# Performance work log

Measured on AMD Instinct MI355X. Metric: run time of the kernel, lower is better.

The kernel has to match this reference:

```python
import jax, jax.numpy as jnp
import numpy as np

N_HEADS, D_MODEL, D_HEAD = 12, 768, 64
INIT_RANGE = 0.02
IGNORE = -100000.0

def setup_inputs() -> dict:
    key = jax.random.key(0)
    ks = jax.random.split(key, 5)
    x = jax.random.normal(ks[0], (4, 2048, D_MODEL), dtype=jnp.float32)
    W_Q = jax.random.normal(ks[1], (N_HEADS, D_MODEL, D_HEAD), dtype=jnp.float32) * INIT_RANGE
    W_K = jax.random.normal(ks[2], (N_HEADS, D_MODEL, D_HEAD), dtype=jnp.float32) * INIT_RANGE
    W_V = jax.random.normal(ks[3], (N_HEADS, D_MODEL, D_HEAD), dtype=jnp.float32) * INIT_RANGE
    W_O = jax.random.normal(ks[4], (N_HEADS, D_HEAD, D_MODEL), dtype=jnp.float32) * INIT_RANGE
    b_Q = jnp.zeros((N_HEADS, D_HEAD), dtype=jnp.float32)
    b_K = jnp.zeros((N_HEADS, D_HEAD), dtype=jnp.float32)
    b_V = jnp.zeros((N_HEADS, D_HEAD), dtype=jnp.float32)
    b_O = jnp.zeros((D_MODEL,), dtype=jnp.float32)
    return {"normalized_resid_pre": x, "W_Q": W_Q, "b_Q": b_Q, "W_K": W_K,
            "b_K": b_K, "W_V": W_V, "b_V": b_V, "W_O": W_O, "b_O": b_O}

def reference(normalized_resid_pre, W_Q, b_Q, W_K, b_K, W_V, b_V, W_O, b_O):
    x = normalized_resid_pre  # [b, s, d_model]
    q = jnp.einsum('bsd,hde->bshe', x, W_Q) + b_Q  # [b, s, h, d_head]
    k = jnp.einsum('bsd,hde->bshe', x, W_K) + b_K
    v = jnp.einsum('bsd,hde->bshe', x, W_V) + b_V
    scores = jnp.einsum('bqhe,bkhe->bhqk', q, k) / jnp.sqrt(jnp.float32(D_HEAD))
    S = x.shape[1]
    causal = jnp.triu(jnp.ones((S, S), dtype=bool), k=1)  # True above diagonal
    scores = jnp.where(causal, jnp.float32(IGNORE), scores)
    pattern = jax.nn.softmax(scores, axis=-1)  # [b, h, q, k]
    z = jnp.einsum('bhqk,bkhe->bqhe', pattern, v)
    attn_out = jnp.einsum('bqhe,hed->bqd', z, W_O) + b_O
    return attn_out
```

## Files before the change

### kernel.cpp

```cpp
#include <hip/hip_runtime.h>

typedef unsigned short u16;
typedef __bf16 bf16x8 __attribute__((ext_vector_type(8)));
typedef float f32x4 __attribute__((ext_vector_type(4)));

#define D_MODEL 768
#define NH 12
#define SEQ 2048
#define BB 4
#define QSCALE 0.18033688011112042f
#define FIXM 8.0f

__device__ __forceinline__ u16 f2b(float f) {
  __bf16 h = (__bf16)f;
  return __builtin_bit_cast(u16, h);
}

__device__ __forceinline__ void gload16(const void* g, void* l) {
  __builtin_amdgcn_global_load_lds((__attribute__((address_space(1))) void*)g,
                                   (__attribute__((address_space(3))) void*)l, 16, 0, 0);
}

__device__ __forceinline__ f32x4 mm16(bf16x8 a, bf16x8 b, f32x4 c) {
  return __builtin_amdgcn_mfma_f32_16x16x32_bf16(a, b, c, 0, 0, 0);
}

__global__ void prep_kernel(const float* __restrict__ x, const float* __restrict__ wq,
                            const float* __restrict__ wk, const float* __restrict__ wv,
                            const float* __restrict__ wo, const float* __restrict__ bq,
                            const float* __restrict__ bk, const float* __restrict__ bv,
                            u16* __restrict__ xb, u16* __restrict__ wt,
                            u16* __restrict__ wot, float* __restrict__ qkvb) {
  const int bid = blockIdx.x;
  if (bid < 6144) {
    int i = (bid * 256 + threadIdx.x) * 4;
    float4 v = *(const float4*)&x[i];
    ushort4 o;
    o.x = f2b(v.x); o.y = f2b(v.y); o.z = f2b(v.z); o.w = f2b(v.w);
    *(ushort4*)&xb[i] = o;
  } else {
    int i = (bid - 6144) * 256 + threadIdx.x;
    {
      int cp = i / 768, d = i % 768;
      int proj = cp / 768, c = cp % 768, h = c / 64, e = c % 64;
      const float* W = (proj == 0) ? wq : ((proj == 1) ? wk : wv);
      float v = W[(size_t)h * 49152 + d * 64 + e];
      if (proj == 0) v *= QSCALE;
      wt[i] = f2b(v);
    }
    if (i < 768 * 768) {
      int rp = i / 768, d = i % 768;
      wot[i] = f2b(wo[(size_t)d * 768 + rp]);
    }
    if (i < 2304) {
      int proj = i / 768, c = i % 768;
      float v = (proj == 0) ? bq[c] * QSCALE : ((proj == 1) ? bk[c] : bv[c]);
      qkvb[i] = v;
    }
  }
}

__global__ __launch_bounds__(512) void gemm_qkv_kernel(
    const u16* __restrict__ A, const u16* __restrict__ Bt,
    const float* __restrict__ qkvb, u16* __restrict__ qw, u16* __restrict__ kw,
    u16* __restrict__ vw) {
  __shared__ u16 lds[73728];
  const int tid = threadIdx.x;
  const int w = tid >> 6, lane = tid & 63;
  const int lg = lane >> 4, cl = lane & 15;
  const int L = blockIdx.x;
  const int v = (L & 7) * 72 + (L >> 3);
  const int bm = v % 9, bn = v / 9;
  const int wr = w >> 1, wc = w & 1;
  const int NT = 12;

  f32x4 vzero = {0.f, 0.f, 0.f, 0.f};
  f32x4 acc[4][4];
#pragma unroll
  for (int mi = 0; mi < 4; mi++)
#pragma unroll
    for (int ni = 0; ni < 4; ni++) acc[mi][ni] = vzero;

  const u16* aB = A + (size_t)bm * 256 * D_MODEL;
  const u16* bB = Bt + (size_t)bn * 128 * D_MODEL;
  const int l8 = lane >> 3, l7 = lane & 7;

  auto stage = [&](int buf, int kt, int half) {
    const int kof = kt * 64;
#pragma unroll
    for (int j2 = 0; j2 < 2; j2++) {
      const int r0 = (w * 4 + half * 2 + j2) * 8;
      gload16(aB + (size_t)(r0 + l8) * D_MODEL + kof + l7 * 8,
              &lds[buf * 16384 + r0 * 64]);
    }
    const int r0b = (w * 2 + half) * 8;
    gload16(bB + (size_t)(r0b + l8) * D_MODEL + kof + l7 * 8,
            &lds[49152 + buf * 8192 + r0b * 64]);
  };

  stage(0, 0, 0); stage(0, 0, 1);
  stage(1, 1, 0); stage(1, 1, 1);
  asm volatile("s_waitcnt vmcnt(6)" ::: "memory");
  __builtin_amdgcn_s_barrier();

  for (int kt = 0; kt < NT; ++kt) {
    const int cA = (kt % 3) * 16384;
    const int cB = 49152 + (kt % 3) * 8192;
    const int nbuf = (kt + 2) % 3;
#pragma unroll
    for (int ks = 0; ks < 2; ks++) {
      bf16x8 af[4], bf4[4];
#pragma unroll
      for (int mi = 0; mi < 4; mi++)
        af[mi] = *(const bf16x8*)&lds[cA + (wr * 64 + mi * 16 + cl) * 64 + ks * 32 + lg * 8];
#pragma unroll
      for (int ni = 0; ni < 4; ni++)
        bf4[ni] = *(const bf16x8*)&lds[cB + (wc * 64 + ni * 16 + cl) * 64 + ks * 32 + lg * 8];
      if (kt + 2 < NT) stage(nbuf, kt + 2, ks);
      if (ks == 1) {
        if (kt + 2 < NT) asm volatile("s_waitcnt vmcnt(6)" ::: "memory");
        else asm volatile("s_waitcnt vmcnt(0)" ::: "memory");
      }
      __builtin_amdgcn_s_barrier();
      __builtin_amdgcn_s_setprio(1);
#pragma unroll
      for (int mi = 0; mi < 4; mi++)
#pragma unroll
        for (int ni = 0; ni < 4; ni++)
          acc[mi][ni] = mm16(af[mi], bf4[ni], acc[mi][ni]);
      __builtin_amdgcn_s_setprio(0);
      __builtin_amdgcn_s_barrier();
    }
  }

  __syncthreads();
  u16* lw = &lds[w * 4096];
  const int cm = bm * 256 + wr * 64;
  const int cn = bn * 128 + wc * 64;
  const int proj = cm / 768;
  const int h = (cm % 768) >> 6;
  const int b = cn >> 11, s_base = cn & 2047;
  const int rlo = lane >> 3, q8 = lane & 7;

  float bz[4][4];
#pragma unroll
  for (int mi = 0; mi < 4; mi++) {
    float4 b4 = *(const float4*)&qkvb[cm + mi * 16 + lg * 4];
    bz[mi][0] = b4.x; bz[mi][1] = b4.y; bz[mi][2] = b4.z; bz[mi][3] = b4.w;
  }

  if (proj < 2) {
#pragma unroll
    for (int mi = 0; mi < 4; mi++) {
      const int e0 = mi * 16 + lg * 4;
#pragma unroll
      for (int ni = 0; ni < 4; ni++) {
        const int s_l = ni * 16 + cl;
        ushort4 pk;
        pk.x = f2b(acc[mi][ni][0] + bz[mi][0]);
        pk.y = f2b(acc[mi][ni][1] + bz[mi][1]);
        pk.z = f2b(acc[mi][ni][2] + bz[mi][2]);
        pk.w = f2b(acc[mi][ni][3] + bz[mi][3]);
        *(ushort4*)&lw[(s_l * 128 + ((e0 * 2) ^ ((s_l & 7) << 4))) >> 1] = pk;
      }
    }
    u16* dst = ((proj == 0) ? qw : kw) + (((size_t)(b * NH + h) * SEQ + s_base) << 6);
#pragma unroll
    for (int it = 0; it < 8; it++) {
      const int row = it * 8 + rlo;
      *(bf16x8*)&dst[row * 64 + q8 * 8] =
          *(const bf16x8*)&lw[(row * 128 + ((q8 * 16) ^ ((row & 7) << 4))) >> 1];
    }
  } else {
#pragma unroll
    for (int mi = 0; mi < 4; mi++)
#pragma unroll
      for (int ni = 0; ni < 4; ni++) {
        const int s_l = ni * 16 + cl;
#pragma unroll
        for (int r = 0; r < 4; r++) {
          const int e_l = mi * 16 + lg * 4 + r;
          lw[(e_l * 128 + ((s_l * 2) ^ ((e_l & 7) << 4))) >> 1] =
              f2b(acc[mi][ni][r] + bz[mi][r]);
        }
      }
    u16* dst = vw + (((size_t)(b * NH + h)) << 17) + s_base;
#pragma unroll
    for (int it = 0; it < 8; it++) {
      const int row = it * 8 + rlo;
      *(bf16x8*)&dst[((size_t)row << 11) + q8 * 8] =
          *(const bf16x8*)&lw[(row * 128 + ((q8 * 16) ^ ((row & 7) << 4))) >> 1];
    }
  }
}

__global__ __launch_bounds__(256) void gemm_out_kernel(
    const u16* __restrict__ A, const u16* __restrict__ Bt,
    const float* __restrict__ bias0, float* __restrict__ outf) {
  __shared__ u16 lds[16384];
  const int tid = threadIdx.x;
  const int w = tid >> 6, lane = tid & 63;
  const int lg = lane >> 4, cl = lane & 15;
  const int L = blockIdx.x;
  const int v = (L & 7) * 48 + (L >> 3);
  const int bn = v % 6, bm = v / 6;
  const int wr = w >> 1, wc = w & 1;
  const int NK = D_MODEL / 32;

  f32x4 vzero = {0.f, 0.f, 0.f, 0.f};
  f32x4 acc[4][4];
#pragma unroll
  for (int mi = 0; mi < 4; mi++)
#pragma unroll
    for (int ni = 0; ni < 4; ni++) acc[mi][ni] = vzero;

  const u16* aB = A + (size_t)bm * 128 * D_MODEL;
  const u16* bB = Bt + (size_t)bn * 128 * D_MODEL;

  auto stage = [&](int buf, int kt) {
    const int kof = kt * 32 + w * 8;
    gload16(aB + (size_t)(lane)*D_MODEL + kof, &lds[buf * 4096 + (w * 128 + 0) * 8]);
    gload16(aB + (size_t)(64 + lane) * D_MODEL + kof,
            &lds[buf * 4096 + (w * 128 + 64) * 8]);
    gload16(bB + (size_t)(lane)*D_MODEL + kof,
            &lds[8192 + buf * 4096 + (w * 128 + 0) * 8]);
    gload16(bB + (size_t)(64 + lane) * D_MODEL + kof,
            &lds[8192 + buf * 4096 + (w * 128 + 64) * 8]);
  };

  stage(0, 0);
  stage(1, 1);
  for (int kt = 0; kt < NK; ++kt) {
    const int cur = kt & 1;
    if (kt < NK - 1) asm volatile("s_waitcnt vmcnt(4)" ::: "memory");
    else asm volatile("s_waitcnt vmcnt(0)" ::: "memory");
    __builtin_amdgcn_s_barrier();

    bf16x8 af[4], bf4[4];
#pragma unroll
    for (int mi = 0; mi < 4; mi++)
      af[mi] = *(const bf16x8*)&lds[cur * 4096 + (lg * 128 + wr * 64 + mi * 16 + cl) * 8];
#pragma unroll
    for (int ni = 0; ni < 4; ni++)
      bf4[ni] = *(const bf16x8*)&lds[8192 + cur * 4096 +
                                     (lg * 128 + wc * 64 + ni * 16 + cl) * 8];
    __builtin_amdgcn_s_setprio(1);
#pragma unroll
    for (int mi = 0; mi < 4; mi++)
#pragma unroll
      for (int ni = 0; ni < 4; ni++)
        acc[mi][ni] = mm16(af[mi], bf4[ni], acc[mi][ni]);
    __builtin_amdgcn_s_setprio(0);

    asm volatile("s_waitcnt lgkmcnt(0)" ::: "memory");
    __builtin_amdgcn_s_barrier();
    if (kt + 2 < NK) stage(cur, kt + 2);
  }

  __syncthreads();
  u16* lw = &lds[w * 4096];
  float* lwf = (float*)lw;
  const int m_base = bm * 128 + wr * 64;
  const int n0 = bn * 128 + wc * 64;
  const int rlo = lane >> 3, q8 = lane & 7;
#pragma unroll
  for (int hh = 0; hh < 2; hh++) {
#pragma unroll
    for (int nn = 0; nn < 2; nn++) {
      const int ni = hh * 2 + nn;
      const float bz = bias0[n0 + ni * 16 + cl];
      const int col = nn * 16 + cl;
#pragma unroll
      for (int mi = 0; mi < 4; mi++)
#pragma unroll
        for (int r = 0; r < 4; r++) {
          const int row = mi * 16 + lg * 4 + r;
          lwf[(row * 128 + ((col * 4) ^ ((row & 7) << 4))) >> 2] = acc[mi][ni][r] + bz;
        }
    }
#pragma unroll
    for (int it = 0; it < 8; it++) {
      const int row = it * 8 + rlo;
      const int byt = row * 128 + ((q8 * 16) ^ ((row & 7) << 4));
      *(float4*)&outf[(size_t)(m_base + row) * D_MODEL + n0 + hh * 32 + q8 * 4] =
          *(const float4*)((const char*)lwf + byt);
    }
  }
}

__global__ __launch_bounds__(256) void attn_kernel(
    const u16* __restrict__ q_ws, const u16* __restrict__ k_ws,
    const u16* __restrict__ vT_ws, u16* __restrict__ z_ws) {
  __shared__ u16 lk[2][4096];
  __shared__ u16 lv[2][4096];
  __shared__ u16 lp[4096];
  const int tid = threadIdx.x, w = tid >> 6, lane = tid & 63;
  const int lg = lane >> 4, cl = lane & 15, c7 = cl & 7;
  const int L = blockIdx.x;
  const int vv = (L & 7) * 96 + (L >> 3);
  const int pair = vv & 15, bh = vv >> 4;
  const u16* qp = q_ws + (size_t)bh * SEQ * 64;
  const u16* kp = k_ws + (size_t)bh * SEQ * 64;
  const u16* vp = vT_ws + (size_t)bh * 64 * SEQ;
  const int b = bh / NH, h = bh % NH;

  for (int sel = 0; sel < 2; ++sel) {
    const int qt = (sel == 0) ? pair : 31 - pair;
    const int q0 = qt * 64;
    const int qabs = q0 + w * 16 + cl;

    bf16x8 qf[2];
#pragma unroll
    for (int ks = 0; ks < 2; ks++)
      qf[ks] = *(const bf16x8*)&qp[(size_t)(q0 + w * 16 + cl) * 64 + ks * 32 + lg * 8];

    f32x4 vzero = {0.f, 0.f, 0.f, 0.f};
    f32x4 accO[4];
#pragma unroll
    for (int nb = 0; nb < 4; nb++) accO[nb] = vzero;
    float lrun = 0.f;

#pragma unroll
    for (int c2 = 0; c2 < 2; c2++) {
      const int ch = w + c2 * 4;
      gload16(kp + (size_t)(lane)*64 + ch * 8, &lk[0][ch * 64 * 8]);
      gload16(vp + (size_t)lane * SEQ + ch * 8, &lv[0][ch * 64 * 8]);
    }
    asm volatile("s_waitcnt vmcnt(0)" ::: "memory");
    __builtin_amdgcn_s_barrier();

    for (int kt = 0; kt <= qt; ++kt) {
      const int cur = kt & 1;
      const int k0 = kt * 64;
      if (kt < qt) {
        const int kn = k0 + 64;
#pragma unroll
        for (int c2 = 0; c2 < 2; c2++) {
          const int ch = w + c2 * 4;
          gload16(kp + (size_t)(kn + lane) * 64 + ch * 8, &lk[cur ^ 1][ch * 64 * 8]);
          gload16(vp + (size_t)lane * SEQ + kn + ch * 8, &lv[cur ^ 1][ch * 64 * 8]);
        }
      }

      f32x4 sa[4];
#pragma unroll
      for (int cb = 0; cb < 4; cb++) sa[cb] = vzero;
      __builtin_amdgcn_s_setprio(1);
#pragma unroll
      for (int ks = 0; ks < 2; ks++) {
#pragma unroll
        for (int cb = 0; cb < 4; cb++) {
          bf16x8 kf = *(const bf16x8*)&lk[cur][((ks * 4 + lg) * 64 + cb * 16 + cl) * 8];
          sa[cb] = mm16(kf, qf[ks], sa[cb]);
        }
      }
      __builtin_amdgcn_s_setprio(0);
      if (kt == qt) {
#pragma unroll
        for (int cb = 0; cb < 4; cb++)
#pragma unroll
          for (int r = 0; r < 4; r++)
            if (k0 + cb * 16 + lg * 4 + r > qabs) sa[cb][r] = -1e30f;
      }

      float ps = 0.f;
#pragma unroll
      for (int cb = 0; cb < 4; cb++) {
        float p0 = __builtin_amdgcn_exp2f(sa[cb][0] - FIXM);
        float p1 = __builtin_amdgcn_exp2f(sa[cb][1] - FIXM);
        float p2 = __builtin_amdgcn_exp2f(sa[cb][2] - FIXM);
        float p3 = __builtin_amdgcn_exp2f(sa[cb][3] - FIXM);
        ps += (p0 + p1) + (p2 + p3);
        ushort4 pk;
        pk.x = f2b(p0); pk.y = f2b(p1); pk.z = f2b(p2); pk.w = f2b(p3);
        *(ushort4*)&lp[w * 1024 + (cl * 128 + ((cb * 32 + lg * 8) ^ (c7 << 4))) / 2] = pk;
      }
      ps += __shfl_xor(ps, 16);
      ps += __shfl_xor(ps, 32);
      lrun += ps;

      __builtin_amdgcn_s_setprio(1);
#pragma unroll
      for (int ks = 0; ks < 2; ks++) {
        bf16x8 pf = *(const bf16x8*)&lp[w * 1024 +
                                        (cl * 128 + ((ks * 64 + lg * 16) ^ (c7 << 4))) / 2];
#pragma unroll
        for (int nb = 0; nb < 4; nb++) {
          bf16x8 vf = *(const bf16x8*)&lv[cur][((ks * 4 + lg) * 64 + nb * 16 + cl) * 8];
          accO[nb] = mm16(pf, vf, accO[nb]);
        }
      }
      __builtin_amdgcn_s_setprio(0);

      asm volatile("s_waitcnt vmcnt(0)" ::: "memory");
      __builtin_amdgcn_s_barrier();
    }

    float inv[4];
#pragma unroll
    for (int r = 0; r < 4; r++) inv[r] = 1.f / __shfl(lrun, lg * 4 + r);
#pragma unroll
    for (int nb = 0; nb < 4; nb++)
#pragma unroll
      for (int r = 0; r < 4; r++) {
        const int qrow = q0 + w * 16 + lg * 4 + r;
        z_ws[((size_t)b * SEQ + qrow) * D_MODEL + h * 64 + nb * 16 + cl] =
            f2b(accO[nb][r] * inv[r]);
      }
  }
}

extern "C" void kernel_launch(void* const* d_in, const int* in_sizes, int n_in,
                              void* d_out, int out_size, void* d_ws, size_t ws_size,
                              hipStream_t stream) {
  const float* x = (const float*)d_in[0];
  const float* wq = (const float*)d_in[1];
  const float* bq = (const float*)d_in[2];
  const float* wk = (const float*)d_in[3];
  const float* bk = (const float*)d_in[4];
  const float* wv = (const float*)d_in[5];
  const float* bv = (const float*)d_in[6];
  const float* wo = (const float*)d_in[7];
  const float* bo = (const float*)d_in[8];
  float* out = (float*)d_out;

  char* ws = (char*)d_ws;
  size_t off = 0;
  auto carve = [&](size_t bytes) -> u16* {
    u16* p = (u16*)(ws + off);
    off += (bytes + 255) & ~(size_t)255;
    return p;
  };
  u16* xb = carve((size_t)8192 * 768 * 2);
  u16* wt = carve((size_t)2304 * 768 * 2);
  u16* wot = carve((size_t)768 * 768 * 2);
  float* qkvb = (float*)carve((size_t)2304 * 4);
  u16* qw = carve((size_t)BB * NH * SEQ * 64 * 2);
  u16* kw = carve((size_t)BB * NH * SEQ * 64 * 2);
  u16* vw = carve((size_t)BB * NH * SEQ * 64 * 2);
  u16* zw = carve((size_t)8192 * 768 * 2);
  if (ws_size < off) return;

  prep_kernel<<<dim3(13056), dim3(256), 0, stream>>>(x, wq, wk, wv, wo, bq, bk, bv,
                                                     xb, wt, wot, qkvb);
  gemm_qkv_kernel<<<dim3(576), dim3(512), 0, stream>>>(wt, xb, qkvb, qw, kw, vw);
  attn_kernel<<<dim3(768), dim3(256), 0, stream>>>(qw, kw, vw, zw);
  gemm_out_kernel<<<dim3(384), dim3(256), 0, stream>>>(zw, wot, bo, out);
}
```

Measured before the change: 158.8 us.

## Enlarge output GEMM tiles with triple-buffered pipeline; compute softmax rowsum via MFMA

The output projection GEMM now uses 256x128 tiles with 512 threads, a 64-wide K step and a three-stage LDS buffer that has loads interleaved between MFMA half-steps. This halves the grid and increases operand reuse per block. The cost is a much larger LDS footprint (144 KB) and lower occupancy. In the attention kernel, the softmax denominator is now accumulated by an extra MFMA against a vector of ones, replacing the per-tile scalar adds and cross-lane shuffles. That row sum is built from the bf16-rounded probabilities, so it matches the values used in the P·V product.

```diff
diff --git a/kernel.cpp b/kernel.cpp
--- a/kernel.cpp
+++ b/kernel.cpp
@@ -194,18 +194,18 @@
   }
 }
 
-__global__ __launch_bounds__(256) void gemm_out_kernel(
+__global__ __launch_bounds__(512) void gemm_out_kernel(
     const u16* __restrict__ A, const u16* __restrict__ Bt,
     const float* __restrict__ bias0, float* __restrict__ outf) {
-  __shared__ u16 lds[16384];
+  __shared__ u16 lds[73728];
   const int tid = threadIdx.x;
   const int w = tid >> 6, lane = tid & 63;
   const int lg = lane >> 4, cl = lane & 15;
   const int L = blockIdx.x;
-  const int v = (L & 7) * 48 + (L >> 3);
-  const int bn = v % 6, bm = v / 6;
+  const int v = (L & 7) * 24 + (L >> 3);
+  const int bm = v / 6, bn = v % 6;
   const int wr = w >> 1, wc = w & 1;
-  const int NK = D_MODEL / 32;
+  const int NT = 12;
 
   f32x4 vzero = {0.f, 0.f, 0.f, 0.f};
   f32x4 acc[4][4];
@@ -214,53 +214,62 @@
 #pragma unroll
     for (int ni = 0; ni < 4; ni++) acc[mi][ni] = vzero;
 
-  const u16* aB = A + (size_t)bm * 128 * D_MODEL;
+  const u16* aB = A + (size_t)bm * 256 * D_MODEL;
   const u16* bB = Bt + (size_t)bn * 128 * D_MODEL;
-
-  auto stage = [&](int buf, int kt) {
-    const int kof = kt * 32 + w * 8;
-    gload16(aB + (size_t)(lane)*D_MODEL + kof, &lds[buf * 4096 + (w * 128 + 0) * 8]);
-    gload16(aB + (size_t)(64 + lane) * D_MODEL + kof,
-            &lds[buf * 4096 + (w * 128 + 64) * 8]);
-    gload16(bB + (size_t)(lane)*D_MODEL + kof,
-            &lds[8192 + buf * 4096 + (w * 128 + 0) * 8]);
-    gload16(bB + (size_t)(64 + lane) * D_MODEL + kof,
-            &lds[8192 + buf * 4096 + (w * 128 + 64) * 8]);
+  const int l8 = lane >> 3, l7 = lane & 7;
+
+  auto stage = [&](int buf, int kt, int half) {
+    const int kof = kt * 64;
+#pragma unroll
+    for (int j2 = 0; j2 < 2; j2++) {
+      const int r0 = (w * 4 + half * 2 + j2) * 8;
+      gload16(aB + (size_t)(r0 + l8) * D_MODEL + kof + l7 * 8,
+              &lds[buf * 16384 + r0 * 64]);
+    }
+    const int r0b = (w * 2 + half) * 8;
+    gload16(bB + (size_t)(r0b + l8) * D_MODEL + kof + l7 * 8,
+            &lds[49152 + buf * 8192 + r0b * 64]);
   };
 
-  stage(0, 0);
-  stage(1, 1);
-  for (int kt = 0; kt < NK; ++kt) {
-    const int cur = kt & 1;
-    if (kt < NK - 1) asm volatile("s_waitcnt vmcnt(4)" ::: "memory");
-    else asm volatile("s_waitcnt vmcnt(0)" ::: "memory");
-    __builtin_amdgcn_s_barrier();
-
-    bf16x8 af[4], bf4[4];
-#pragma unroll
-    for (int mi = 0; mi < 4; mi++)
-      af[mi] = *(const bf16x8*)&lds[cur * 4096 + (lg * 128 + wr * 64 + mi * 16 + cl) * 8];
-#pragma unroll
-    for (int ni = 0; ni < 4; ni++)
-      bf4[ni] = *(const bf16x8*)&lds[8192 + cur * 4096 +
-                                     (lg * 128 + wc * 64 + ni * 16 + cl) * 8];
-    __builtin_amdgcn_s_setprio(1);
-#pragma unroll
-    for (int mi = 0; mi < 4; mi++)
+  stage(0, 0, 0); stage(0, 0, 1);
+  stage(1, 1, 0); stage(1, 1, 1);
+  asm volatile("s_waitcnt vmcnt(6)" ::: "memory");
+  __builtin_amdgcn_s_barrier();
+
+  for (int kt = 0; kt < NT; ++kt) {
+    const int cA = (kt % 3) * 16384;
+    const int cB = 49152 + (kt % 3) * 8192;
+    const int nbuf = (kt + 2) % 3;
+#pragma unroll
+    for (int ks = 0; ks < 2; ks++) {
+      bf16x8 af[4], bf4[4];
+#pragma unroll
+      for (int mi = 0; mi < 4; mi++)
+        af[mi] = *(const bf16x8*)&lds[cA + (wr * 64 + mi * 16 + cl) * 64 + ks * 32 + lg * 8];
 #pragma unroll
       for (int ni = 0; ni < 4; ni++)
-        acc[mi][ni] = mm16(af[mi], bf4[ni], acc[mi][ni]);
-    __builtin_amdgcn_s_setprio(0);
-
-    asm volatile("s_waitcnt lgkmcnt(0)" ::: "memory");
-    __builtin_amdgcn_s_barrier();
-    if (kt + 2 < NK) stage(cur, kt + 2);
+        bf4[ni] = *(const bf16x8*)&lds[cB + (wc * 64 + ni * 16 + cl) * 64 + ks * 32 + lg * 8];
+      if (kt + 2 < NT) stage(nbuf, kt + 2, ks);
+      if (ks == 1) {
+        if (kt + 2 < NT) asm volatile("s_waitcnt vmcnt(6)" ::: "memory");
+        else asm volatile("s_waitcnt vmcnt(0)" ::: "memory");
+      }
+      __builtin_amdgcn_s_barrier();
+      __builtin_amdgcn_s_setprio(1);
+#pragma unroll
+      for (int mi = 0; mi < 4; mi++)
+#pragma unroll
+        for (int ni = 0; ni < 4; ni++)
+          acc[mi][ni] = mm16(af[mi], bf4[ni], acc[mi][ni]);
+      __builtin_amdgcn_s_setprio(0);
+      __builtin_amdgcn_s_barrier();
+    }
   }
 
   __syncthreads();
   u16* lw = &lds[w * 4096];
   float* lwf = (float*)lw;
-  const int m_base = bm * 128 + wr * 64;
+  const int m_base = bm * 256 + wr * 64;
   const int n0 = bn * 128 + wc * 64;
   const int rlo = lane >> 3, q8 = lane & 7;
 #pragma unroll
@@ -304,6 +313,9 @@
   const u16* vp = vT_ws + (size_t)bh * 64 * SEQ;
   const int b = bh / NH, h = bh % NH;
 
+  const __bf16 one1 = (__bf16)1.0f;
+  const bf16x8 vones = {one1, one1, one1, one1, one1, one1, one1, one1};
+
   for (int sel = 0; sel < 2; ++sel) {
     const int qt = (sel == 0) ? pair : 31 - pair;
     const int q0 = qt * 64;
@@ -318,7 +330,7 @@
     f32x4 accO[4];
 #pragma unroll
     for (int nb = 0; nb < 4; nb++) accO[nb] = vzero;
-    float lrun = 0.f;
+    f32x4 accS = vzero;
 
 #pragma unroll
     for (int c2 = 0; c2 < 2; c2++) {
@@ -363,21 +375,16 @@
             if (k0 + cb * 16 + lg * 4 + r > qabs) sa[cb][r] = -1e30f;
       }
 
-      float ps = 0.f;
 #pragma unroll
       for (int cb = 0; cb < 4; cb++) {
         float p0 = __builtin_amdgcn_exp2f(sa[cb][0] - FIXM);
         float p1 = __builtin_amdgcn_exp2f(sa[cb][1] - FIXM);
         float p2 = __builtin_amdgcn_exp2f(sa[cb][2] - FIXM);
         float p3 = __builtin_amdgcn_exp2f(sa[cb][3] - FIXM);
-        ps += (p0 + p1) + (p2 + p3);
         ushort4 pk;
         pk.x = f2b(p0); pk.y = f2b(p1); pk.z = f2b(p2); pk.w = f2b(p3);
         *(ushort4*)&lp[w * 1024 + (cl * 128 + ((cb * 32 + lg * 8) ^ (c7 << 4))) / 2] = pk;
       }
-      ps += __shfl_xor(ps, 16);
-      ps += __shfl_xor(ps, 32);
-      lrun += ps;
 
       __builtin_amdgcn_s_setprio(1);
 #pragma unroll
@@ -389,6 +396,7 @@
           bf16x8 vf = *(const bf16x8*)&lv[cur][((ks * 4 + lg) * 64 + nb * 16 + cl) * 8];
           accO[nb] = mm16(pf, vf, accO[nb]);
         }
+        accS = mm16(pf, vones, accS);
       }
       __builtin_amdgcn_s_setprio(0);
 
@@ -398,7 +406,7 @@
 
     float inv[4];
 #pragma unroll
-    for (int r = 0; r < 4; r++) inv[r] = 1.f / __shfl(lrun, lg * 4 + r);
+    for (int r = 0; r < 4; r++) inv[r] = 1.f / accS[r];
 #pragma unroll
     for (int nb = 0; nb < 4; nb++)
 #pragma unroll
@@ -445,5 +453,5 @@
                                                      xb, wt, wot, qkvb);
   gemm_qkv_kernel<<<dim3(576), dim3(512), 0, stream>>>(wt, xb, qkvb, qw, kw, vw);
   attn_kernel<<<dim3(768), dim3(256), 0, stream>>>(qw, kw, vw, zw);
-  gemm_out_kernel<<<dim3(384), dim3(256), 0, stream>>>(zw, wot, bo, out);
-}
+  gemm_out_kernel<<<dim3(192), dim3(512), 0, stream>>>(zw, wot, bo, out);
+}
```

Result: faster. 151.0 us (-4.9%).
